# Kernel optimization log

Hardware: AMD Instinct MI355X
Metric: run time of the kernel (lower is better)

The kernel has to match this reference:

```python
import math
import jax, jax.numpy as jnp
import numpy as np

BATCH, LENGTH, D_MODEL, D_STATE = 8, 2048, 1024, 64
DT_MIN, DT_MAX = 1e-3, 1e-1


def setup_inputs() -> dict:
    key = jax.random.key(0)
    k1, k2, k3, k4 = jax.random.split(key, 4)
    x = jax.random.normal(k1, (BATCH, LENGTH, D_MODEL), dtype=jnp.float32)
    # dt_init == 'random': log_dt ~ U[log(dt_min), log(dt_max)], dt_scale = 1.0
    log_dt = jax.random.uniform(k2, (D_MODEL,), dtype=jnp.float32) * (
        math.log(DT_MAX) - math.log(DT_MIN)) + math.log(DT_MIN)
    scale = 1.0 / math.sqrt(D_STATE)
    B = jax.random.normal(k3, (D_MODEL, D_STATE), dtype=jnp.float32) * scale
    C = jax.random.normal(k4, (D_MODEL, D_STATE), dtype=jnp.float32) * scale
    D = jnp.ones((D_MODEL,), dtype=jnp.float32)
    return {"x": x, "log_dt": log_dt, "B": B, "C": C, "D": D}


def reference(x, log_dt, B, C, D):
    """S4DKernel.forward(x, mode='conv') -> y of shape [batch, length, d_model]."""
    d_model, d_state = B.shape
    length = x.shape[1]
    # A buffer: -0.5 * [1..d_state]
    A = -0.5 * jnp.arange(1, d_state + 1, dtype=jnp.float32)  # [N]
    # ZOH discretization
    dt = jnp.exp(log_dt)                       # [D]
    dtA = dt[:, None] * A[None, :]             # [D, N]
    A_bar = jnp.exp(dtA)                       # [D, N]
    B_bar = jnp.expm1(dtA) / A[None, :] * B    # [D, N]
    # Vandermonde kernel: K[d, k] = sum_n C[d,n] * B_bar[d,n] * A_bar[d,n]^k
    k_range = jnp.arange(length, dtype=jnp.float32)                 # [L]
    log_A_bar = jnp.log(jnp.clip(A_bar, 1e-10))                     # [D, N]
    powers = jnp.exp(log_A_bar[:, :, None] * k_range[None, None, :])  # [D, N, L]
    kernel = jnp.einsum('dn,dnk->dk', C * B_bar, powers)            # [D, L]
    # FFT convolution (linear conv via 2L-point FFT)
    x_t = jnp.swapaxes(x, 1, 2)                # [B, D, L]
    fft_size = 2 * length
    x_f = jnp.fft.rfft(x_t, n=fft_size)        # [B, D, L+1]
    k_f = jnp.fft.rfft(kernel, n=fft_size)     # [D, L+1]
    y = jnp.fft.irfft(x_f * k_f[None], n=fft_size)[..., :length]
    y = y + D[None, :, None] * x_t             # skip connection
    return jnp.swapaxes(y, 1, 2)               # [B, L, D]
```

## Files before the change

### kernel.cpp

```cpp
#include <hip/hip_runtime.h>
#include <math.h>


namespace {
constexpr int kBatch = 8;
constexpr int kLen   = 2048;
constexpr int kD     = 1024;
constexpr int kN     = 64;
constexpr int kT     = 64;
constexpr int kC     = kLen / kT;

constexpr long kU     = (long)kBatch * kC * kN * kD;
constexpr long kAOff  = kU;
constexpr long kCbOff = kAOff + (long)kN * kD;
constexpr long kAtOff = kCbOff + (long)kN * kD;
}

__global__ void s4d_coef_kernel(const float* __restrict__ log_dt,
                                const float* __restrict__ Bm,
                                const float* __restrict__ Cm,
                                float* __restrict__ ws) {
  int tid = blockIdx.x * blockDim.x + threadIdx.x;
  int d = tid & (kD - 1);
  int n = tid >> 10;
  float dt  = expf(log_dt[d]);
  float An  = -0.5f * (float)(n + 1);
  float dtA = dt * An;
  float a   = expf(dtA);
  float bbar = (expm1f(dtA) / An) * Bm[d * kN + n];
  float cb   = Cm[d * kN + n] * bbar;
  float aT   = expf(dtA * (float)kT);
  ws[kAOff  + (long)n * kD + d] = a;
  ws[kCbOff + (long)n * kD + d] = cb;
  ws[kAtOff + (long)n * kD + d] = aT;
}

__global__ __launch_bounds__(256) void s4d_state_kernel(
    const float* __restrict__ x, float* __restrict__ ws) {
  constexpr int NG = 8;
  int tid = blockIdx.x * blockDim.x + threadIdx.x;
  int d  = tid & (kD - 1);
  int bc = tid >> 10;
  int b  = bc >> 5;
  int c  = bc & (kC - 1);

  const float* xp = x + ((long)b * kLen + (long)c * kT) * kD + d;
  float xv[kT];
#pragma unroll
  for (int t = 0; t < kT; ++t) xv[t] = xp[(long)t * kD];

  const float* ap = ws + kAOff + d;
  float* up = ws + ((long)bc * kN) * kD + d;
#pragma unroll 1
  for (int g = 0; g < kN; g += NG) {
    float a[NG], h[NG];
#pragma unroll
    for (int i = 0; i < NG; ++i) {
      a[i] = ap[(long)(g + i) * kD];
      h[i] = 0.f;
    }
#pragma unroll
    for (int t = 0; t < kT; ++t) {
      float xt = xv[t];
#pragma unroll
      for (int i = 0; i < NG; ++i) h[i] = fmaf(h[i], a[i], xt);
    }
#pragma unroll
    for (int i = 0; i < NG; ++i) up[(long)(g + i) * kD] = h[i];
  }
}

__global__ void s4d_scan_kernel(float* __restrict__ ws) {
  int tid = blockIdx.x * blockDim.x + threadIdx.x;
  int d  = tid & (kD - 1);
  int bn = tid >> 10;
  int n  = bn & (kN - 1);
  int b  = bn >> 6;
  float aT = ws[kAtOff + (long)n * kD + d];
  float* up = ws + ((long)b * kC * kN + n) * kD + d;
  const long cstride = (long)kN * kD;
  float s = 0.f;
#pragma unroll 1
  for (int c = 0; c < kC; ++c) {
    float u = up[(long)c * cstride];
    up[(long)c * cstride] = s;
    s = fmaf(aT, s, u);
  }
}

__global__ __launch_bounds__(256, 2) void s4d_out_kernel(
    const float* __restrict__ x, const float* __restrict__ Dv,
    float* __restrict__ y, const float* __restrict__ ws) {
  constexpr int NG = 8;
  int tid = blockIdx.x * blockDim.x + threadIdx.x;
  int d  = tid & (kD - 1);
  int bc = tid >> 10;
  int b  = bc >> 5;
  int c  = bc & (kC - 1);

  const float* xp = x + ((long)b * kLen + (long)c * kT) * kD + d;
  float xv[kT];
#pragma unroll
  for (int t = 0; t < kT; ++t) xv[t] = xp[(long)t * kD];

  float Dd = Dv[d];
  float acc[kT];
#pragma unroll
  for (int t = 0; t < kT; ++t) acc[t] = Dd * xv[t];

  const float* ap  = ws + kAOff + d;
  const float* cbp = ws + kCbOff + d;
  const float* sp  = ws + ((long)bc * kN) * kD + d;

#pragma unroll 1
  for (int g = 0; g < kN; g += NG) {
    float a[NG], cb[NG], h[NG];
#pragma unroll
    for (int i = 0; i < NG; ++i) {
      long o = (long)(g + i) * kD;
      a[i]  = ap[o];
      cb[i] = cbp[o];
      h[i]  = sp[o];
    }
#pragma unroll
    for (int t = 0; t < kT; ++t) {
      float xt = xv[t];
      float s  = acc[t];
#pragma unroll
      for (int i = 0; i < NG; ++i) {
        h[i] = fmaf(h[i], a[i], xt);
        s    = fmaf(cb[i], h[i], s);
      }
      acc[t] = s;
    }
  }

  float* yp = y + ((long)b * kLen + (long)c * kT) * kD + d;
#pragma unroll
  for (int t = 0; t < kT; ++t) yp[(long)t * kD] = acc[t];
}

extern "C" void kernel_launch(void* const* d_in, const int* in_sizes, int n_in,
                              void* d_out, int out_size, void* d_ws,
                              size_t ws_size, hipStream_t stream) {
  const float* x      = (const float*)d_in[0];
  const float* log_dt = (const float*)d_in[1];
  const float* Bm     = (const float*)d_in[2];
  const float* Cm     = (const float*)d_in[3];
  const float* Dv     = (const float*)d_in[4];
  float* y  = (float*)d_out;
  float* ws = (float*)d_ws;

  hipLaunchKernelGGL(s4d_coef_kernel, dim3((kN * kD) / 256), dim3(256), 0,
                     stream, log_dt, Bm, Cm, ws);
  hipLaunchKernelGGL(s4d_state_kernel, dim3((kBatch * kC * kD) / 256),
                     dim3(256), 0, stream, x, ws);
  hipLaunchKernelGGL(s4d_scan_kernel, dim3((kBatch * kN * kD) / 256),
                     dim3(256), 0, stream, ws);
  hipLaunchKernelGGL(s4d_out_kernel, dim3((kBatch * kC * kD) / 256),
                     dim3(256), 0, stream, x, Dv, y, ws);
}
```

Before: 223.2 us.

## Split output chunks into half-chunks with mid-chunk state carry

```diff
diff --git a/kernel.cpp b/kernel.cpp
--- a/kernel.cpp
+++ b/kernel.cpp
@@ -9,9 +9,11 @@
 constexpr int kN     = 64;
 constexpr int kT     = 64;
 constexpr int kC     = kLen / kT;
+constexpr int kTO    = 32;
 
-constexpr long kU     = (long)kBatch * kC * kN * kD;
-constexpr long kAOff  = kU;
+constexpr long kHalf  = (long)kBatch * kC * kN * kD;
+constexpr long kUMid  = kHalf;
+constexpr long kAOff  = 2 * kHalf;
 constexpr long kCbOff = kAOff + (long)kN * kD;
 constexpr long kAtOff = kCbOff + (long)kN * kD;
 }
@@ -50,7 +52,8 @@
   for (int t = 0; t < kT; ++t) xv[t] = xp[(long)t * kD];
 
   const float* ap = ws + kAOff + d;
-  float* up = ws + ((long)bc * kN) * kD + d;
+  float* u64p  = ws + ((long)bc * kN) * kD + d;
+  float* umidp = u64p + kUMid;
 #pragma unroll 1
   for (int g = 0; g < kN; g += NG) {
     float a[NG], h[NG];
@@ -60,13 +63,21 @@
       h[i] = 0.f;
     }
 #pragma unroll
-    for (int t = 0; t < kT; ++t) {
+    for (int t = 0; t < kTO; ++t) {
       float xt = xv[t];
 #pragma unroll
       for (int i = 0; i < NG; ++i) h[i] = fmaf(h[i], a[i], xt);
     }
 #pragma unroll
-    for (int i = 0; i < NG; ++i) up[(long)(g + i) * kD] = h[i];
+    for (int i = 0; i < NG; ++i) umidp[(long)(g + i) * kD] = h[i];
+#pragma unroll
+    for (int t = kTO; t < kT; ++t) {
+      float xt = xv[t];
+#pragma unroll
+      for (int i = 0; i < NG; ++i) h[i] = fmaf(h[i], a[i], xt);
+    }
+#pragma unroll
+    for (int i = 0; i < NG; ++i) u64p[(long)(g + i) * kD] = h[i];
   }
 }
 
@@ -76,41 +87,48 @@
   int bn = tid >> 10;
   int n  = bn & (kN - 1);
   int b  = bn >> 6;
-  float aT = ws[kAtOff + (long)n * kD + d];
-  float* up = ws + ((long)b * kC * kN + n) * kD + d;
+  float aT  = ws[kAtOff + (long)n * kD + d];
+  float a32 = sqrtf(aT);
+  float* u64p  = ws + ((long)b * kC * kN + n) * kD + d;
+  float* umidp = u64p + kUMid;
   const long cstride = (long)kN * kD;
   float s = 0.f;
 #pragma unroll 1
   for (int c = 0; c < kC; ++c) {
-    float u = up[(long)c * cstride];
-    up[(long)c * cstride] = s;
+    float u = u64p[(long)c * cstride];
+    float m = umidp[(long)c * cstride];
+    u64p[(long)c * cstride]  = s;
+    umidp[(long)c * cstride] = fmaf(a32, s, m);
     s = fmaf(aT, s, u);
   }
 }
 
-__global__ __launch_bounds__(256, 2) void s4d_out_kernel(
+__global__ __launch_bounds__(256, 3) void s4d_out_kernel(
     const float* __restrict__ x, const float* __restrict__ Dv,
     float* __restrict__ y, const float* __restrict__ ws) {
   constexpr int NG = 8;
   int tid = blockIdx.x * blockDim.x + threadIdx.x;
   int d  = tid & (kD - 1);
-  int bc = tid >> 10;
-  int b  = bc >> 5;
-  int c  = bc & (kC - 1);
+  int j  = tid >> 10;
+  int b  = j >> 6;
+  int r  = j & 63;
+  int c  = r >> 1;
+  int hc = r & 1;
 
-  const float* xp = x + ((long)b * kLen + (long)c * kT) * kD + d;
-  float xv[kT];
+  const float* xp =
+      x + ((long)b * kLen + (long)c * kT + (long)hc * kTO) * kD + d;
+  float xv[kTO];
 #pragma unroll
-  for (int t = 0; t < kT; ++t) xv[t] = xp[(long)t * kD];
+  for (int t = 0; t < kTO; ++t) xv[t] = xp[(long)t * kD];
 
   float Dd = Dv[d];
-  float acc[kT];
+  float acc[kTO];
 #pragma unroll
-  for (int t = 0; t < kT; ++t) acc[t] = Dd * xv[t];
+  for (int t = 0; t < kTO; ++t) acc[t] = Dd * xv[t];
 
   const float* ap  = ws + kAOff + d;
   const float* cbp = ws + kCbOff + d;
-  const float* sp  = ws + ((long)bc * kN) * kD + d;
+  const float* sp  = ws + (long)hc * kUMid + ((long)(b * kC + c) * kN) * kD + d;
 
 #pragma unroll 1
   for (int g = 0; g < kN; g += NG) {
@@ -123,7 +141,7 @@
       h[i]  = sp[o];
     }
 #pragma unroll
-    for (int t = 0; t < kT; ++t) {
+    for (int t = 0; t < kTO; ++t) {
       float xt = xv[t];
       float s  = acc[t];
 #pragma unroll
@@ -135,9 +153,9 @@
     }
   }
 
-  float* yp = y + ((long)b * kLen + (long)c * kT) * kD + d;
+  float* yp = y + ((long)b * kLen + (long)c * kT + (long)hc * kTO) * kD + d;
 #pragma unroll
-  for (int t = 0; t < kT; ++t) yp[(long)t * kD] = acc[t];
+  for (int t = 0; t < kTO; ++t) yp[(long)t * kD] = acc[t];
 }
 
 extern "C" void kernel_launch(void* const* d_in, const int* in_sizes, int n_in,
@@ -157,6 +175,6 @@
                      dim3(256), 0, stream, x, ws);
   hipLaunchKernelGGL(s4d_scan_kernel, dim3((kBatch * kN * kD) / 256),
                      dim3(256), 0, stream, ws);
-  hipLaunchKernelGGL(s4d_out_kernel, dim3((kBatch * kC * kD) / 256),
+  hipLaunchKernelGGL(s4d_out_kernel, dim3((kBatch * 2 * kC * kD) / 256),
                      dim3(256), 0, stream, x, Dv, y, ws);
 }
```

Measured after the change: 250.2 us. 12.1% more time.

## Split output chunk across two warp roles with LDS-pipelined state handoff

Applied to the files above, without the earlier changes.

```diff
diff --git a/kernel.cpp b/kernel.cpp
--- a/kernel.cpp
+++ b/kernel.cpp
@@ -9,6 +9,9 @@
 constexpr int kN     = 64;
 constexpr int kT     = 64;
 constexpr int kC     = kLen / kT;
+constexpr int kTO    = 32;
+constexpr int kNG    = 8;
+constexpr int kG     = kN / kNG;
 
 constexpr long kU     = (long)kBatch * kC * kN * kD;
 constexpr long kAOff  = kU;
@@ -37,14 +40,11 @@
 
 __global__ __launch_bounds__(256) void s4d_state_kernel(
     const float* __restrict__ x, float* __restrict__ ws) {
-  constexpr int NG = 8;
   int tid = blockIdx.x * blockDim.x + threadIdx.x;
   int d  = tid & (kD - 1);
   int bc = tid >> 10;
-  int b  = bc >> 5;
-  int c  = bc & (kC - 1);
 
-  const float* xp = x + ((long)b * kLen + (long)c * kT) * kD + d;
+  const float* xp = x + ((long)bc * kT) * kD + d;
   float xv[kT];
 #pragma unroll
   for (int t = 0; t < kT; ++t) xv[t] = xp[(long)t * kD];
@@ -52,10 +52,10 @@
   const float* ap = ws + kAOff + d;
   float* up = ws + ((long)bc * kN) * kD + d;
 #pragma unroll 1
-  for (int g = 0; g < kN; g += NG) {
-    float a[NG], h[NG];
+  for (int g = 0; g < kN; g += kNG) {
+    float a[kNG], h[kNG];
 #pragma unroll
-    for (int i = 0; i < NG; ++i) {
+    for (int i = 0; i < kNG; ++i) {
       a[i] = ap[(long)(g + i) * kD];
       h[i] = 0.f;
     }
@@ -63,10 +63,10 @@
     for (int t = 0; t < kT; ++t) {
       float xt = xv[t];
 #pragma unroll
-      for (int i = 0; i < NG; ++i) h[i] = fmaf(h[i], a[i], xt);
+      for (int i = 0; i < kNG; ++i) h[i] = fmaf(h[i], a[i], xt);
     }
 #pragma unroll
-    for (int i = 0; i < NG; ++i) up[(long)(g + i) * kD] = h[i];
+    for (int i = 0; i < kNG; ++i) up[(long)(g + i) * kD] = h[i];
   }
 }
 
@@ -88,56 +88,91 @@
   }
 }
 
-__global__ __launch_bounds__(256, 2) void s4d_out_kernel(
+__global__ __launch_bounds__(256, 3) void s4d_out_kernel(
     const float* __restrict__ x, const float* __restrict__ Dv,
     float* __restrict__ y, const float* __restrict__ ws) {
-  constexpr int NG = 8;
-  int tid = blockIdx.x * blockDim.x + threadIdx.x;
-  int d  = tid & (kD - 1);
-  int bc = tid >> 10;
-  int b  = bc >> 5;
-  int c  = bc & (kC - 1);
+  __shared__ float hbuf[2][kNG][128];
 
-  const float* xp = x + ((long)b * kLen + (long)c * kT) * kD + d;
-  float xv[kT];
+  int tidx = threadIdx.x;
+  int role = tidx >> 7;
+  int dloc = tidx & 127;
+  int blk  = blockIdx.x;
+  int dblk = blk & 7;
+  int bc   = blk >> 3;
+  int d    = dblk * 128 + dloc;
+
+  const float* xp =
+      x + ((long)bc * kT + (long)role * kTO) * kD + d;
+  float xv[kTO];
 #pragma unroll
-  for (int t = 0; t < kT; ++t) xv[t] = xp[(long)t * kD];
+  for (int t = 0; t < kTO; ++t) xv[t] = xp[(long)t * kD];
 
   float Dd = Dv[d];
-  float acc[kT];
+  float acc[kTO];
 #pragma unroll
-  for (int t = 0; t < kT; ++t) acc[t] = Dd * xv[t];
+  for (int t = 0; t < kTO; ++t) acc[t] = Dd * xv[t];
 
   const float* ap  = ws + kAOff + d;
   const float* cbp = ws + kCbOff + d;
   const float* sp  = ws + ((long)bc * kN) * kD + d;
 
 #pragma unroll 1
-  for (int g = 0; g < kN; g += NG) {
-    float a[NG], cb[NG], h[NG];
+  for (int p = 0; p <= kG; ++p) {
+    if (p > 0) __syncthreads();
+    if (role == 0) {
+      if (p < kG) {
+        int g = p * kNG;
+        float a[kNG], cb[kNG], h[kNG];
 #pragma unroll
-    for (int i = 0; i < NG; ++i) {
-      long o = (long)(g + i) * kD;
-      a[i]  = ap[o];
-      cb[i] = cbp[o];
-      h[i]  = sp[o];
-    }
+        for (int i = 0; i < kNG; ++i) {
+          long o = (long)(g + i) * kD;
+          a[i]  = ap[o];
+          cb[i] = cbp[o];
+          h[i]  = sp[o];
+        }
 #pragma unroll
-    for (int t = 0; t < kT; ++t) {
-      float xt = xv[t];
-      float s  = acc[t];
+        for (int t = 0; t < kTO; ++t) {
+          float xt = xv[t];
+          float s  = acc[t];
 #pragma unroll
-      for (int i = 0; i < NG; ++i) {
-        h[i] = fmaf(h[i], a[i], xt);
-        s    = fmaf(cb[i], h[i], s);
+          for (int i = 0; i < kNG; ++i) {
+            h[i] = fmaf(h[i], a[i], xt);
+            s    = fmaf(cb[i], h[i], s);
+          }
+          acc[t] = s;
+        }
+#pragma unroll
+        for (int i = 0; i < kNG; ++i) hbuf[p & 1][i][dloc] = h[i];
       }
-      acc[t] = s;
+    } else {
+      if (p > 0) {
+        int g = (p - 1) * kNG;
+        float a[kNG], cb[kNG], h[kNG];
+#pragma unroll
+        for (int i = 0; i < kNG; ++i) {
+          long o = (long)(g + i) * kD;
+          a[i]  = ap[o];
+          cb[i] = cbp[o];
+          h[i]  = hbuf[(p - 1) & 1][i][dloc];
+        }
+#pragma unroll
+        for (int t = 0; t < kTO; ++t) {
+          float xt = xv[t];
+          float s  = acc[t];
+#pragma unroll
+          for (int i = 0; i < kNG; ++i) {
+            h[i] = fmaf(h[i], a[i], xt);
+            s    = fmaf(cb[i], h[i], s);
+          }
+          acc[t] = s;
+        }
+      }
     }
   }
 
-  float* yp = y + ((long)b * kLen + (long)c * kT) * kD + d;
+  float* yp = y + ((long)bc * kT + (long)role * kTO) * kD + d;
 #pragma unroll
-  for (int t = 0; t < kT; ++t) yp[(long)t * kD] = acc[t];
+  for (int t = 0; t < kTO; ++t) yp[(long)t * kD] = acc[t];
 }
 
 extern "C" void kernel_launch(void* const* d_in, const int* in_sizes, int n_in,
@@ -157,6 +192,6 @@
                      dim3(256), 0, stream, x, ws);
   hipLaunchKernelGGL(s4d_scan_kernel, dim3((kBatch * kN * kD) / 256),
                      dim3(256), 0, stream, ws);
-  hipLaunchKernelGGL(s4d_out_kernel, dim3((kBatch * kC * kD) / 256),
+  hipLaunchKernelGGL(s4d_out_kernel, dim3(kBatch * kC * (kD / 128)),
                      dim3(256), 0, stream, x, Dv, y, ws);
 }
```

Result: slower. 235.3 us (+5.4%).

## Halve chunk length and store chunk states in bf16 to cut traffic

Applied to the files above, without the earlier changes.

```diff
diff --git a/kernel.cpp b/kernel.cpp
--- a/kernel.cpp
+++ b/kernel.cpp
@@ -7,13 +7,26 @@
 constexpr int kLen   = 2048;
 constexpr int kD     = 1024;
 constexpr int kN     = 64;
-constexpr int kT     = 64;
+constexpr int kT     = 32;
 constexpr int kC     = kLen / kT;
+constexpr int kNG    = 8;
 
-constexpr long kU     = (long)kBatch * kC * kN * kD;
-constexpr long kAOff  = kU;
+constexpr long kUElems = (long)kBatch * kC * kN * kD;
+constexpr long kAOff  = kUElems / 2;
 constexpr long kCbOff = kAOff + (long)kN * kD;
 constexpr long kAtOff = kCbOff + (long)kN * kD;
+
+__device__ __forceinline__ float bf2f(unsigned short v) {
+  union { unsigned int u; float f; } c;
+  c.u = (unsigned int)v << 16;
+  return c.f;
+}
+__device__ __forceinline__ unsigned short f2bf(float f) {
+  union { unsigned int u; float f; } c;
+  c.f = f;
+  unsigned int u = c.u + 0x7FFFu + ((c.u >> 16) & 1u);
+  return (unsigned short)(u >> 16);
+}
 }
 
 __global__ void s4d_coef_kernel(const float* __restrict__ log_dt,
@@ -37,25 +50,22 @@
 
 __global__ __launch_bounds__(256) void s4d_state_kernel(
     const float* __restrict__ x, float* __restrict__ ws) {
-  constexpr int NG = 8;
   int tid = blockIdx.x * blockDim.x + threadIdx.x;
   int d  = tid & (kD - 1);
   int bc = tid >> 10;
-  int b  = bc >> 5;
-  int c  = bc & (kC - 1);
 
-  const float* xp = x + ((long)b * kLen + (long)c * kT) * kD + d;
+  const float* xp = x + ((long)bc * kT) * kD + d;
   float xv[kT];
 #pragma unroll
   for (int t = 0; t < kT; ++t) xv[t] = xp[(long)t * kD];
 
   const float* ap = ws + kAOff + d;
-  float* up = ws + ((long)bc * kN) * kD + d;
+  unsigned short* up = (unsigned short*)ws + ((long)bc * kN) * kD + d;
 #pragma unroll 1
-  for (int g = 0; g < kN; g += NG) {
-    float a[NG], h[NG];
+  for (int g = 0; g < kN; g += kNG) {
+    float a[kNG], h[kNG];
 #pragma unroll
-    for (int i = 0; i < NG; ++i) {
+    for (int i = 0; i < kNG; ++i) {
       a[i] = ap[(long)(g + i) * kD];
       h[i] = 0.f;
     }
@@ -63,10 +73,10 @@
     for (int t = 0; t < kT; ++t) {
       float xt = xv[t];
 #pragma unroll
-      for (int i = 0; i < NG; ++i) h[i] = fmaf(h[i], a[i], xt);
+      for (int i = 0; i < kNG; ++i) h[i] = fmaf(h[i], a[i], xt);
     }
 #pragma unroll
-    for (int i = 0; i < NG; ++i) up[(long)(g + i) * kD] = h[i];
+    for (int i = 0; i < kNG; ++i) up[(long)(g + i) * kD] = f2bf(h[i]);
   }
 }
 
@@ -77,28 +87,26 @@
   int n  = bn & (kN - 1);
   int b  = bn >> 6;
   float aT = ws[kAtOff + (long)n * kD + d];
-  float* up = ws + ((long)b * kC * kN + n) * kD + d;
+  unsigned short* up =
+      (unsigned short*)ws + ((long)b * kC * kN + n) * kD + d;
   const long cstride = (long)kN * kD;
   float s = 0.f;
 #pragma unroll 1
   for (int c = 0; c < kC; ++c) {
-    float u = up[(long)c * cstride];
-    up[(long)c * cstride] = s;
+    float u = bf2f(up[(long)c * cstride]);
+    up[(long)c * cstride] = f2bf(s);
     s = fmaf(aT, s, u);
   }
 }
 
-__global__ __launch_bounds__(256, 2) void s4d_out_kernel(
+__global__ __launch_bounds__(256, 3) void s4d_out_kernel(
     const float* __restrict__ x, const float* __restrict__ Dv,
     float* __restrict__ y, const float* __restrict__ ws) {
-  constexpr int NG = 8;
   int tid = blockIdx.x * blockDim.x + threadIdx.x;
   int d  = tid & (kD - 1);
-  int bc = tid >> 10;
-  int b  = bc >> 5;
-  int c  = bc & (kC - 1);
+  int j  = tid >> 10;
 
-  const float* xp = x + ((long)b * kLen + (long)c * kT) * kD + d;
+  const float* xp = x + ((long)j * kT) * kD + d;
   float xv[kT];
 #pragma unroll
   for (int t = 0; t < kT; ++t) xv[t] = xp[(long)t * kD];
@@ -110,24 +118,25 @@
 
   const float* ap  = ws + kAOff + d;
   const float* cbp = ws + kCbOff + d;
-  const float* sp  = ws + ((long)bc * kN) * kD + d;
+  const unsigned short* sp =
+      (const unsigned short*)ws + ((long)j * kN) * kD + d;
 
 #pragma unroll 1
-  for (int g = 0; g < kN; g += NG) {
-    float a[NG], cb[NG], h[NG];
+  for (int g = 0; g < kN; g += kNG) {
+    float a[kNG], cb[kNG], h[kNG];
 #pragma unroll
-    for (int i = 0; i < NG; ++i) {
+    for (int i = 0; i < kNG; ++i) {
       long o = (long)(g + i) * kD;
       a[i]  = ap[o];
       cb[i] = cbp[o];
-      h[i]  = sp[o];
+      h[i]  = bf2f(sp[o]);
     }
 #pragma unroll
     for (int t = 0; t < kT; ++t) {
       float xt = xv[t];
       float s  = acc[t];
 #pragma unroll
-      for (int i = 0; i < NG; ++i) {
+      for (int i = 0; i < kNG; ++i) {
         h[i] = fmaf(h[i], a[i], xt);
         s    = fmaf(cb[i], h[i], s);
       }
@@ -135,7 +144,7 @@
     }
   }
 
-  float* yp = y + ((long)b * kLen + (long)c * kT) * kD + d;
+  float* yp = y + ((long)j * kT) * kD + d;
 #pragma unroll
   for (int t = 0; t < kT; ++t) yp[(long)t * kD] = acc[t];
 }
```

New measurement: 226.8 us. About the same (+1.6%).
